# Kernel optimization log

Measured on AMD Instinct MI355X. Metric: run time of the kernel, lower is better.

The kernel has to match this reference:

```python
import jax, jax.numpy as jnp
import numpy as np

N = 50000      # nodes
E = 400000     # edges (before self-loops)
NFEAT = 256
NHID = 64
NHEAD = 8
NOUT = 128


def gat_conv(h, src, dst, W, attn_l, attn_r, bias, n, H, D):
    """DGL GATConv (eval mode: feat_drop/attn_drop are no-ops), negative_slope=0.2."""
    feat = (h @ W).reshape(n, H, D)                      # [N,H,D]
    el = jnp.einsum('nhd,hd->nh', feat, attn_l)          # [N,H]
    er = jnp.einsum('nhd,hd->nh', feat, attn_r)          # [N,H]
    e = jax.nn.leaky_relu(el[src] + er[dst], 0.2)        # [E,H]
    # segment softmax over incoming edges of each dst node
    m = jax.ops.segment_max(e, dst, num_segments=n)      # [N,H] (every node has a self-loop)
    ex = jnp.exp(e - m[dst])
    denom = jax.ops.segment_sum(ex, dst, num_segments=n)
    a = ex / denom[dst]                                  # [E,H]
    rst = jax.ops.segment_sum(a[:, :, None] * feat[src], dst, num_segments=n)  # [N,H,D]
    return rst + bias.reshape(1, H, D)


def setup_inputs() -> dict:
    key = jax.random.key(0)
    ks = jax.random.split(key, 10)
    s = 0.1
    x = jax.random.normal(ks[0], (N, NFEAT), jnp.float32)
    edge_index = jax.random.randint(ks[1], (2, E), 0, N, dtype=jnp.int64)
    W1 = jax.random.normal(ks[2], (NFEAT, NHEAD * NHID), jnp.float32) * s
    al1 = jax.random.normal(ks[3], (NHEAD, NHID), jnp.float32) * s
    ar1 = jax.random.normal(ks[4], (NHEAD, NHID), jnp.float32) * s
    b1 = jax.random.normal(ks[5], (NHEAD * NHID,), jnp.float32) * s
    W2 = jax.random.normal(ks[6], (NHEAD * NHID, NOUT), jnp.float32) * s
    al2 = jax.random.normal(ks[7], (1, NOUT), jnp.float32) * s
    ar2 = jax.random.normal(ks[8], (1, NOUT), jnp.float32) * s
    b2 = jax.random.normal(ks[9], (NOUT,), jnp.float32) * s
    return {"x": x, "edge_index": edge_index, "W1": W1, "al1": al1, "ar1": ar1,
            "b1": b1, "W2": W2, "al2": al2, "ar2": ar2, "b2": b2}


def reference(x, edge_index, W1, al1, ar1, b1, W2, al2, ar2, b2):
    n = x.shape[0]
    loop = jnp.arange(n, dtype=edge_index.dtype)
    src = jnp.concatenate([edge_index[0], loop])  # dgl.add_self_loop
    dst = jnp.concatenate([edge_index[1], loop])
    # hidden layer (dropout is identity in eval mode)
    h = gat_conv(x, src, dst, W1, al1, ar1, b1, n, NHEAD, NHID).reshape(n, NFEAT * 2)
    h = jax.nn.elu(h)
    out = gat_conv(h, src, dst, W2, al2, ar2, b2, n, 1, NOUT).reshape(n, NOUT)
    return out
```

## Files before the change

kernel.cpp:

```cpp
#include <hip/hip_runtime.h>

#define NFEAT 256
#define NHID 64
#define NHEAD 8
#define HID1 512
#define NOUT 128

typedef unsigned short ushort_t;
typedef unsigned int uint_t;
typedef __attribute__((ext_vector_type(8))) short short8;
typedef __attribute__((ext_vector_type(4))) float floatx4;
typedef __attribute__((ext_vector_type(4))) ushort_t ushort4_t;

static __device__ __forceinline__ float bf2f(uint_t s) {
    return __uint_as_float(s << 16);
}
static __device__ __forceinline__ ushort_t f2bf(float f) {
    uint_t u = __float_as_uint(f);
    u += 0x7FFF + ((u >> 16) & 1);
    return (ushort_t)(u >> 16);
}

__global__ void k_prep(const float* __restrict__ x, ushort_t* __restrict__ xb,
                       const float* __restrict__ W1, ushort_t* __restrict__ W1t,
                       const float* __restrict__ W2, ushort_t* __restrict__ W2t,
                       const int* __restrict__ dstA, int* __restrict__ deg,
                       int n, int E, int c0, int c1, int c2) {
    int blk = blockIdx.x;
    int t = threadIdx.x;
    if (blk < c0) {
        int i = blk * 256 + t;
        floatx4 f = ((const floatx4*)x)[i];
        ushort4_t o;
        #pragma unroll
        for (int j = 0; j < 4; ++j) o[j] = f2bf(f[j]);
        ((ushort4_t*)xb)[i] = o;
    } else if (blk < c1) {
        int i = (blk - c0) * 256 + t;
        int nn = i / NFEAT, kk = i % NFEAT;
        W1t[i] = f2bf(W1[(size_t)kk * HID1 + nn]);
    } else if (blk < c2) {
        int i = (blk - c1) * 256 + t;
        int nn = i / HID1, kk = i % HID1;
        W2t[i] = f2bf(W2[(size_t)kk * NOUT + nn]);
    } else {
        int i = (blk - c2) * 256 + t;
        if (i < E + n) {
            int d = (i < E) ? dstA[i] : (i - E);
            atomicAdd(&deg[d], 1);
        }
    }
}

__global__ __launch_bounds__(1024) void k_scan(const int* __restrict__ deg, int* __restrict__ indptr, int n) {
    __shared__ int part[1024];
    int t = threadIdx.x;
    int chunk = (n + 1023) >> 10;
    int b = t * chunk;
    int e = min(b + chunk, n);
    int s = 0;
    int i = b;
    for (; i + 3 < e; i += 4)
        s += (deg[i] + deg[i + 1]) + (deg[i + 2] + deg[i + 3]);
    for (; i < e; ++i) s += deg[i];
    part[t] = s;
    __syncthreads();
    for (int off = 1; off < 1024; off <<= 1) {
        int v = (t >= off) ? part[t - off] : 0;
        __syncthreads();
        part[t] += v;
        __syncthreads();
    }
    int run = (t == 0) ? 0 : part[t - 1];
    i = b;
    for (; i + 3 < e; i += 4) {
        int d0 = deg[i], d1 = deg[i + 1], d2 = deg[i + 2], d3 = deg[i + 3];
        indptr[i] = run; run += d0;
        indptr[i + 1] = run; run += d1;
        indptr[i + 2] = run; run += d2;
        indptr[i + 3] = run; run += d3;
    }
    for (; i < e; ++i) { indptr[i] = run; run += deg[i]; }
    if (t == 1023) indptr[n] = part[1023];
}

__global__ void k_fill(const int* __restrict__ srcA, const int* __restrict__ dstA, int E, int n,
                       const int* __restrict__ indptr, int* __restrict__ cnt,
                       int* __restrict__ csr_src, int* __restrict__ csr_dst) {
    int i = blockIdx.x * blockDim.x + threadIdx.x;
    if (i >= E + n) return;
    int s, d;
    if (i < E) { s = srcA[i]; d = dstA[i]; } else { s = i - E; d = s; }
    int pos = indptr[d] + atomicAdd(&cnt[d], 1);
    csr_src[pos] = s;
    csr_dst[pos] = d;
}

__global__ __launch_bounds__(256) void k_gemm1(const ushort_t* __restrict__ A,
                                               const ushort_t* __restrict__ Bt,
                                               ushort_t* __restrict__ C,
                                               const float* __restrict__ al,
                                               const float* __restrict__ ar,
                                               float* __restrict__ el, float* __restrict__ er,
                                               int M) {
    const int N = HID1, K = NFEAT;
    __shared__ __align__(16) ushort_t As[128 * 32];
    __shared__ __align__(16) ushort_t Bs[128 * 32];
    const int t = threadIdx.x;
    const int w = t >> 6, lane = t & 63;
    const int l16 = lane & 15, quad = lane >> 4;
    const int m0 = blockIdx.y * 128, n0 = blockIdx.x * 128;
    const int r0 = (w >> 1) * 64;
    const int c0 = (w & 1) * 64;

    floatx4 acc[4][4] = {};

    const int srow[2] = { (0 * 256 + t) >> 2, (1 * 256 + t) >> 2 };
    const int skp = (t & 3) * 8;
    const int wbase0 = (0 * 256 + (t & ~63)) * 8;
    const int wbase1 = (1 * 256 + (t & ~63)) * 8;

    for (int k0 = 0; k0 < K; k0 += 32) {
        int gr0 = m0 + srow[0]; if (gr0 >= M) gr0 = M - 1;
        int gr1 = m0 + srow[1]; if (gr1 >= M) gr1 = M - 1;
        const ushort_t* gpa0 = A + (size_t)gr0 * K + k0 + skp;
        const ushort_t* gpa1 = A + (size_t)gr1 * K + k0 + skp;
        const ushort_t* gpb0 = Bt + (size_t)(n0 + srow[0]) * K + k0 + skp;
        const ushort_t* gpb1 = Bt + (size_t)(n0 + srow[1]) * K + k0 + skp;
        __builtin_amdgcn_global_load_lds((const __attribute__((address_space(1))) void*)gpa0,
            (__attribute__((address_space(3))) void*)(As + wbase0), 16, 0, 0);
        __builtin_amdgcn_global_load_lds((const __attribute__((address_space(1))) void*)gpa1,
            (__attribute__((address_space(3))) void*)(As + wbase1), 16, 0, 0);
        __builtin_amdgcn_global_load_lds((const __attribute__((address_space(1))) void*)gpb0,
            (__attribute__((address_space(3))) void*)(Bs + wbase0), 16, 0, 0);
        __builtin_amdgcn_global_load_lds((const __attribute__((address_space(1))) void*)gpb1,
            (__attribute__((address_space(3))) void*)(Bs + wbase1), 16, 0, 0);
        __syncthreads();

        short8 af[4], bf[4];
        #pragma unroll
        for (int i = 0; i < 4; ++i)
            af[i] = *(const short8*)(As + (r0 + i * 16 + l16) * 32 + quad * 8);
        #pragma unroll
        for (int j = 0; j < 4; ++j)
            bf[j] = *(const short8*)(Bs + (c0 + j * 16 + l16) * 32 + quad * 8);
        #pragma unroll
        for (int i = 0; i < 4; ++i)
            #pragma unroll
            for (int j = 0; j < 4; ++j)
                acc[i][j] = __builtin_amdgcn_mfma_f32_16x16x32_bf16(af[i], bf[j], acc[i][j], 0, 0, 0);
        __syncthreads();
    }

    #pragma unroll
    for (int i = 0; i < 4; ++i) {
        #pragma unroll
        for (int r = 0; r < 4; ++r) {
            int row = m0 + r0 + i * 16 + quad * 4 + r;
            if (row < M) {
                #pragma unroll
                for (int j = 0; j < 4; ++j)
                    C[(size_t)row * N + n0 + c0 + j * 16 + l16] = f2bf(acc[i][j][r]);
            }
        }
    }

    float alv[4], arv[4];
    #pragma unroll
    for (int j = 0; j < 4; ++j) {
        int col = n0 + c0 + j * 16 + l16;
        alv[j] = al[col];
        arv[j] = ar[col];
    }
    int head = (n0 + c0) >> 6;
    #pragma unroll
    for (int i = 0; i < 4; ++i) {
        #pragma unroll
        for (int r = 0; r < 4; ++r) {
            float p = acc[i][0][r] * alv[0] + acc[i][1][r] * alv[1]
                    + acc[i][2][r] * alv[2] + acc[i][3][r] * alv[3];
            float q = acc[i][0][r] * arv[0] + acc[i][1][r] * arv[1]
                    + acc[i][2][r] * arv[2] + acc[i][3][r] * arv[3];
            #pragma unroll
            for (int o = 8; o > 0; o >>= 1) {
                p += __shfl_down(p, o);
                q += __shfl_down(q, o);
            }
            if (l16 == 0) {
                int row = m0 + r0 + i * 16 + quad * 4 + r;
                if (row < M) {
                    el[row * NHEAD + head] = p;
                    er[row * NHEAD + head] = q;
                }
            }
        }
    }
}

__global__ __launch_bounds__(256) void k_gemm2(const ushort_t* __restrict__ A,
                                               const ushort_t* __restrict__ Bt,
                                               ushort_t* __restrict__ C,
                                               const float* __restrict__ al,
                                               const float* __restrict__ ar,
                                               float* __restrict__ el, float* __restrict__ er,
                                               int M) {
    const int N = NOUT, K = HID1;
    __shared__ __align__(16) ushort_t As[64 * 32];
    __shared__ __align__(16) ushort_t Bs[128 * 32];
    __shared__ float elp[64][2], erp[64][2];
    const int t = threadIdx.x;
    const int w = t >> 6, lane = t & 63;
    const int l16 = lane & 15, quad = lane >> 4;
    const int m0 = blockIdx.y * 64;
    const int r0 = (w >> 1) * 32;
    const int c0 = (w & 1) * 64;

    floatx4 acc[2][4] = {};

    const int arow = t >> 2;
    const int brow[2] = { (0 * 256 + t) >> 2, (1 * 256 + t) >> 2 };
    const int skp = (t & 3) * 8;
    const int wbaseA = (t & ~63) * 8;
    const int wbase0 = (0 * 256 + (t & ~63)) * 8;
    const int wbase1 = (1 * 256 + (t & ~63)) * 8;

    for (int k0 = 0; k0 < K; k0 += 32) {
        int gr = m0 + arow; if (gr >= M) gr = M - 1;
        const ushort_t* gpa = A + (size_t)gr * K + k0 + skp;
        const ushort_t* gpb0 = Bt + (size_t)brow[0] * K + k0 + skp;
        const ushort_t* gpb1 = Bt + (size_t)brow[1] * K + k0 + skp;
        __builtin_amdgcn_global_load_lds((const __attribute__((address_space(1))) void*)gpa,
            (__attribute__((address_space(3))) void*)(As + wbaseA), 16, 0, 0);
        __builtin_amdgcn_global_load_lds((const __attribute__((address_space(1))) void*)gpb0,
            (__attribute__((address_space(3))) void*)(Bs + wbase0), 16, 0, 0);
        __builtin_amdgcn_global_load_lds((const __attribute__((address_space(1))) void*)gpb1,
            (__attribute__((address_space(3))) void*)(Bs + wbase1), 16, 0, 0);
        __syncthreads();

        short8 af[2], bf[4];
        #pragma unroll
        for (int i = 0; i < 2; ++i)
            af[i] = *(const short8*)(As + (r0 + i * 16 + l16) * 32 + quad * 8);
        #pragma unroll
        for (int j = 0; j < 4; ++j)
            bf[j] = *(const short8*)(Bs + (c0 + j * 16 + l16) * 32 + quad * 8);
        #pragma unroll
        for (int i = 0; i < 2; ++i)
            #pragma unroll
            for (int j = 0; j < 4; ++j)
                acc[i][j] = __builtin_amdgcn_mfma_f32_16x16x32_bf16(af[i], bf[j], acc[i][j], 0, 0, 0);
        __syncthreads();
    }

    float alv[4], arv[4];
    #pragma unroll
    for (int j = 0; j < 4; ++j) {
        int col = c0 + j * 16 + l16;
        alv[j] = al[col];
        arv[j] = ar[col];
    }
    #pragma unroll
    for (int i = 0; i < 2; ++i) {
        #pragma unroll
        for (int r = 0; r < 4; ++r) {
            int lrow = r0 + i * 16 + quad * 4 + r;
            int row = m0 + lrow;
            if (row < M) {
                #pragma unroll
                for (int j = 0; j < 4; ++j)
                    C[(size_t)row * N + c0 + j * 16 + l16] = f2bf(acc[i][j][r]);
            }
            float p = acc[i][0][r] * alv[0] + acc[i][1][r] * alv[1]
                    + acc[i][2][r] * alv[2] + acc[i][3][r] * alv[3];
            float q = acc[i][0][r] * arv[0] + acc[i][1][r] * arv[1]
                    + acc[i][2][r] * arv[2] + acc[i][3][r] * arv[3];
            #pragma unroll
            for (int o = 8; o > 0; o >>= 1) {
                p += __shfl_down(p, o);
                q += __shfl_down(q, o);
            }
            if (l16 == 0) {
                elp[lrow][w & 1] = p;
                erp[lrow][w & 1] = q;
            }
        }
    }
    __syncthreads();
    if (t < 64) {
        int row = m0 + t;
        if (row < M) {
            el[row] = elp[t][0] + elp[t][1];
            er[row] = erp[t][0] + erp[t][1];
        }
    }
}

__global__ void k_wgt1(const int* __restrict__ csr_src, const int* __restrict__ csr_dst,
                       const float* __restrict__ el, const float* __restrict__ er,
                       float* __restrict__ wcsr, int ET) {
    int idx = blockIdx.x * blockDim.x + threadIdx.x;
    if (idx >= ET * NHEAD) return;
    int e = idx >> 3, h = idx & 7;
    int s = csr_src[e], d = csr_dst[e];
    float x = el[s * NHEAD + h] + er[d * NHEAD + h];
    x = (x > 0.f) ? x : 0.2f * x;
    wcsr[idx] = __expf(x);
}

__global__ void k_wgt2(const int* __restrict__ csr_src, const int* __restrict__ csr_dst,
                       const float* __restrict__ el2, const float* __restrict__ er2,
                       float* __restrict__ wcsr, int ET) {
    int e = blockIdx.x * blockDim.x + threadIdx.x;
    if (e >= ET) return;
    int s = csr_src[e], d = csr_dst[e];
    float x = el2[s] + er2[d];
    x = (x > 0.f) ? x : 0.2f * x;
    wcsr[e] = __expf(x);
}

__global__ __launch_bounds__(256) void k_agg1(const uint_t* __restrict__ fb, const float* __restrict__ wcsr,
                                              const float* __restrict__ b1,
                                              const int* __restrict__ indptr, const int* __restrict__ csr_src,
                                              uint_t* __restrict__ h1b, int n) {
    int node = blockIdx.x;
    int t = threadIdx.x;
    int h = t >> 5;
    int e0 = indptr[node], e1 = indptr[node + 1];
    float a0 = 0.f, a1 = 0.f, den = 0.f;
    int e = e0;
    for (; e + 3 < e1; e += 4) {
        int s0 = csr_src[e], s1 = csr_src[e + 1], s2 = csr_src[e + 2], s3 = csr_src[e + 3];
        float w0 = wcsr[(size_t)e * NHEAD + h];
        float w1 = wcsr[(size_t)(e + 1) * NHEAD + h];
        float w2 = wcsr[(size_t)(e + 2) * NHEAD + h];
        float w3 = wcsr[(size_t)(e + 3) * NHEAD + h];
        uint_t u0 = fb[(size_t)s0 * 256 + t];
        uint_t u1 = fb[(size_t)s1 * 256 + t];
        uint_t u2 = fb[(size_t)s2 * 256 + t];
        uint_t u3 = fb[(size_t)s3 * 256 + t];
        den += (w0 + w1) + (w2 + w3);
        a0 += w0 * bf2f(u0 & 0xFFFF) + w1 * bf2f(u1 & 0xFFFF)
            + w2 * bf2f(u2 & 0xFFFF) + w3 * bf2f(u3 & 0xFFFF);
        a1 += w0 * bf2f(u0 >> 16) + w1 * bf2f(u1 >> 16)
            + w2 * bf2f(u2 >> 16) + w3 * bf2f(u3 >> 16);
    }
    for (; e < e1; ++e) {
        int s = csr_src[e];
        float w = wcsr[(size_t)e * NHEAD + h];
        uint_t u = fb[(size_t)s * 256 + t];
        den += w;
        a0 += w * bf2f(u & 0xFFFF);
        a1 += w * bf2f(u >> 16);
    }
    float inv = 1.f / den;
    float v0 = a0 * inv + b1[2 * t];
    float v1 = a1 * inv + b1[2 * t + 1];
    v0 = (v0 > 0.f) ? v0 : (__expf(v0) - 1.f);
    v1 = (v1 > 0.f) ? v1 : (__expf(v1) - 1.f);
    h1b[(size_t)node * 256 + t] = (uint_t)f2bf(v0) | ((uint_t)f2bf(v1) << 16);
}

__global__ __launch_bounds__(256) void k_agg2(const uint_t* __restrict__ fb2, const float* __restrict__ wcsr,
                                              const float* __restrict__ b2,
                                              const int* __restrict__ indptr, const int* __restrict__ csr_src,
                                              float* __restrict__ out, int n) {
    int wid = blockIdx.x * 4 + (threadIdx.x >> 6);
    int lane = threadIdx.x & 63;
    if (wid >= n) return;
    int e0 = indptr[wid], e1 = indptr[wid + 1];
    float a0 = 0.f, a1 = 0.f, den = 0.f;
    int e = e0;
    for (; e + 3 < e1; e += 4) {
        int s0 = csr_src[e], s1 = csr_src[e + 1], s2 = csr_src[e + 2], s3 = csr_src[e + 3];
        float w0 = wcsr[e], w1 = wcsr[e + 1], w2 = wcsr[e + 2], w3 = wcsr[e + 3];
        uint_t u0 = fb2[(size_t)s0 * 64 + lane];
        uint_t u1 = fb2[(size_t)s1 * 64 + lane];
        uint_t u2 = fb2[(size_t)s2 * 64 + lane];
        uint_t u3 = fb2[(size_t)s3 * 64 + lane];
        den += (w0 + w1) + (w2 + w3);
        a0 += w0 * bf2f(u0 & 0xFFFF) + w1 * bf2f(u1 & 0xFFFF)
            + w2 * bf2f(u2 & 0xFFFF) + w3 * bf2f(u3 & 0xFFFF);
        a1 += w0 * bf2f(u0 >> 16) + w1 * bf2f(u1 >> 16)
            + w2 * bf2f(u2 >> 16) + w3 * bf2f(u3 >> 16);
    }
    for (; e < e1; ++e) {
        int s = csr_src[e];
        float w = wcsr[e];
        uint_t u = fb2[(size_t)s * 64 + lane];
        den += w;
        a0 += w * bf2f(u & 0xFFFF);
        a1 += w * bf2f(u >> 16);
    }
    float inv = 1.f / den;
    float2 o;
    o.x = a0 * inv + b2[2 * lane];
    o.y = a1 * inv + b2[2 * lane + 1];
    ((float2*)out)[(size_t)wid * 64 + lane] = o;
}

extern "C" void kernel_launch(void* const* d_in, const int* in_sizes, int n_in,
                              void* d_out, int out_size, void* d_ws, size_t ws_size,
                              hipStream_t stream) {
    const float* x   = (const float*)d_in[0];
    const int*   ei  = (const int*)d_in[1];
    const float* W1  = (const float*)d_in[2];
    const float* al1 = (const float*)d_in[3];
    const float* ar1 = (const float*)d_in[4];
    const float* b1  = (const float*)d_in[5];
    const float* W2  = (const float*)d_in[6];
    const float* al2 = (const float*)d_in[7];
    const float* ar2 = (const float*)d_in[8];
    const float* b2  = (const float*)d_in[9];

    const int n  = in_sizes[0] / NFEAT;
    const int E  = in_sizes[1] / 2;
    const int ET = E + n;
    const int* srcA = ei;
    const int* dstA = ei + E;

    char* ws = (char*)d_ws;
    size_t off = 0;
    auto alloc = [&](size_t bytes) -> void* {
        void* p = ws + off;
        off += (bytes + 255) & ~(size_t)255;
        return p;
    };
    ushort_t* xb     = (ushort_t*)alloc((size_t)n * NFEAT * 2);
    ushort_t* feat1b = (ushort_t*)alloc((size_t)n * HID1 * 2);
    ushort_t* h1b    = (ushort_t*)alloc((size_t)n * HID1 * 2);
    ushort_t* feat2b = (ushort_t*)alloc((size_t)n * NOUT * 2);
    ushort_t* W1t    = (ushort_t*)alloc((size_t)NFEAT * HID1 * 2);
    ushort_t* W2t    = (ushort_t*)alloc((size_t)HID1 * NOUT * 2);
    float* el1 = (float*)alloc((size_t)n * NHEAD * 4);
    float* er1 = (float*)alloc((size_t)n * NHEAD * 4);
    float* el2 = (float*)alloc((size_t)n * 4);
    float* er2 = (float*)alloc((size_t)n * 4);
    float* wcsr1 = (float*)alloc((size_t)ET * NHEAD * 4);
    float* wcsr2 = (float*)alloc((size_t)ET * 4);
    int* indptr  = (int*)alloc((size_t)(n + 1) * 4);
    int* deg     = (int*)alloc((size_t)n * 4);
    int* cnt     = (int*)alloc((size_t)n * 4);
    int* csr     = (int*)alloc((size_t)ET * 4);
    int* csrd    = (int*)alloc((size_t)ET * 4);

    hipMemsetAsync(deg, 0, (size_t)n * 4, stream);
    hipMemsetAsync(cnt, 0, (size_t)n * 4, stream);

    const int c0 = (n * NFEAT / 4) / 256;
    const int c1 = c0 + (NFEAT * HID1) / 256;
    const int c2 = c1 + (HID1 * NOUT) / 256;
    const int c3 = c2 + (ET + 255) / 256;
    k_prep<<<c3, 256, 0, stream>>>(x, xb, W1, W1t, W2, W2t, dstA, deg, n, E, c0, c1, c2);

    k_scan<<<1, 1024, 0, stream>>>(deg, indptr, n);
    k_fill<<<(ET + 255) / 256, 256, 0, stream>>>(srcA, dstA, E, n, indptr, cnt, csr, csrd);

    k_gemm1<<<dim3(HID1 / 128, (n + 127) / 128), 256, 0, stream>>>(xb, W1t, feat1b, al1, ar1, el1, er1, n);
    k_wgt1<<<(ET * NHEAD + 255) / 256, 256, 0, stream>>>(csr, csrd, el1, er1, wcsr1, ET);
    k_agg1<<<n, 256, 0, stream>>>((const uint_t*)feat1b, wcsr1, b1, indptr, csr, (uint_t*)h1b, n);

    k_gemm2<<<dim3(1, (n + 63) / 64), 256, 0, stream>>>(h1b, W2t, feat2b, al2, ar2, el2, er2, n);
    k_wgt2<<<(ET + 255) / 256, 256, 0, stream>>>(csr, csrd, el2, er2, wcsr2, ET);
    k_agg2<<<(n + 3) / 4, 256, 0, stream>>>((const uint_t*)feat2b, wcsr2, b2, indptr, csr, (float*)d_out, n);
}
```

Before: 386.7 us.

## Fuse edge-weight computation into aggregation kernels and widen GEMM1 tile

Removes the separate k_wgt1/k_wgt2 kernels and the csr_dst array. Edge attention weights are now computed on the fly inside k_agg1 and k_agg2, staged through shared memory in chunks, which avoids writing and re-reading per-edge weight buffers. GEMM1 now uses a 128x256 tile, so each wave produces two heads' el/er, and the two memsets are merged into one. The cost is extra shared-memory syncs per chunk, more accumulator registers in GEMM1 that may lower occupancy, and exp work that now sits inside the aggregation kernels.

Result: no change. 387.0 us (+0.1%).

```diff
diff --git a/kernel.cpp b/kernel.cpp
--- a/kernel.cpp
+++ b/kernel.cpp
@@ -86,14 +86,13 @@
 
 __global__ void k_fill(const int* __restrict__ srcA, const int* __restrict__ dstA, int E, int n,
                        const int* __restrict__ indptr, int* __restrict__ cnt,
-                       int* __restrict__ csr_src, int* __restrict__ csr_dst) {
+                       int* __restrict__ csr_src) {
     int i = blockIdx.x * blockDim.x + threadIdx.x;
     if (i >= E + n) return;
     int s, d;
     if (i < E) { s = srcA[i]; d = dstA[i]; } else { s = i - E; d = s; }
     int pos = indptr[d] + atomicAdd(&cnt[d], 1);
     csr_src[pos] = s;
-    csr_dst[pos] = d;
 }
 
 __global__ __launch_bounds__(256) void k_gemm1(const ushort_t* __restrict__ A,
@@ -105,49 +104,46 @@
                                                int M) {
     const int N = HID1, K = NFEAT;
     __shared__ __align__(16) ushort_t As[128 * 32];
-    __shared__ __align__(16) ushort_t Bs[128 * 32];
+    __shared__ __align__(16) ushort_t Bs[256 * 32];
     const int t = threadIdx.x;
     const int w = t >> 6, lane = t & 63;
     const int l16 = lane & 15, quad = lane >> 4;
-    const int m0 = blockIdx.y * 128, n0 = blockIdx.x * 128;
+    const int m0 = blockIdx.y * 128, n0 = blockIdx.x * 256;
     const int r0 = (w >> 1) * 64;
-    const int c0 = (w & 1) * 64;
-
-    floatx4 acc[4][4] = {};
-
-    const int srow[2] = { (0 * 256 + t) >> 2, (1 * 256 + t) >> 2 };
+    const int c0 = (w & 1) * 128;
+
+    floatx4 acc[4][8] = {};
+
     const int skp = (t & 3) * 8;
-    const int wbase0 = (0 * 256 + (t & ~63)) * 8;
-    const int wbase1 = (1 * 256 + (t & ~63)) * 8;
-
     for (int k0 = 0; k0 < K; k0 += 32) {
-        int gr0 = m0 + srow[0]; if (gr0 >= M) gr0 = M - 1;
-        int gr1 = m0 + srow[1]; if (gr1 >= M) gr1 = M - 1;
-        const ushort_t* gpa0 = A + (size_t)gr0 * K + k0 + skp;
-        const ushort_t* gpa1 = A + (size_t)gr1 * K + k0 + skp;
-        const ushort_t* gpb0 = Bt + (size_t)(n0 + srow[0]) * K + k0 + skp;
-        const ushort_t* gpb1 = Bt + (size_t)(n0 + srow[1]) * K + k0 + skp;
-        __builtin_amdgcn_global_load_lds((const __attribute__((address_space(1))) void*)gpa0,
-            (__attribute__((address_space(3))) void*)(As + wbase0), 16, 0, 0);
-        __builtin_amdgcn_global_load_lds((const __attribute__((address_space(1))) void*)gpa1,
-            (__attribute__((address_space(3))) void*)(As + wbase1), 16, 0, 0);
-        __builtin_amdgcn_global_load_lds((const __attribute__((address_space(1))) void*)gpb0,
-            (__attribute__((address_space(3))) void*)(Bs + wbase0), 16, 0, 0);
-        __builtin_amdgcn_global_load_lds((const __attribute__((address_space(1))) void*)gpb1,
-            (__attribute__((address_space(3))) void*)(Bs + wbase1), 16, 0, 0);
-        __syncthreads();
-
-        short8 af[4], bf[4];
+        #pragma unroll
+        for (int j = 0; j < 2; ++j) {
+            int r = (j * 256 + t) >> 2;
+            int gr = m0 + r; if (gr >= M) gr = M - 1;
+            const ushort_t* gp = A + (size_t)gr * K + k0 + skp;
+            __builtin_amdgcn_global_load_lds((const __attribute__((address_space(1))) void*)gp,
+                (__attribute__((address_space(3))) void*)(As + (j * 256 + (t & ~63)) * 8), 16, 0, 0);
+        }
+        #pragma unroll
+        for (int j = 0; j < 4; ++j) {
+            int r = (j * 256 + t) >> 2;
+            const ushort_t* gp = Bt + (size_t)(n0 + r) * K + k0 + skp;
+            __builtin_amdgcn_global_load_lds((const __attribute__((address_space(1))) void*)gp,
+                (__attribute__((address_space(3))) void*)(Bs + (j * 256 + (t & ~63)) * 8), 16, 0, 0);
+        }
+        __syncthreads();
+
+        short8 af[4], bf[8];
         #pragma unroll
         for (int i = 0; i < 4; ++i)
             af[i] = *(const short8*)(As + (r0 + i * 16 + l16) * 32 + quad * 8);
         #pragma unroll
-        for (int j = 0; j < 4; ++j)
+        for (int j = 0; j < 8; ++j)
             bf[j] = *(const short8*)(Bs + (c0 + j * 16 + l16) * 32 + quad * 8);
         #pragma unroll
         for (int i = 0; i < 4; ++i)
             #pragma unroll
-            for (int j = 0; j < 4; ++j)
+            for (int j = 0; j < 8; ++j)
                 acc[i][j] = __builtin_amdgcn_mfma_f32_16x16x32_bf16(af[i], bf[j], acc[i][j], 0, 0, 0);
         __syncthreads();
     }
@@ -159,38 +155,46 @@
             int row = m0 + r0 + i * 16 + quad * 4 + r;
             if (row < M) {
                 #pragma unroll
-                for (int j = 0; j < 4; ++j)
+                for (int j = 0; j < 8; ++j)
                     C[(size_t)row * N + n0 + c0 + j * 16 + l16] = f2bf(acc[i][j][r]);
             }
         }
     }
 
-    float alv[4], arv[4];
+    float alv[8], arv[8];
     #pragma unroll
-    for (int j = 0; j < 4; ++j) {
+    for (int j = 0; j < 8; ++j) {
         int col = n0 + c0 + j * 16 + l16;
         alv[j] = al[col];
         arv[j] = ar[col];
     }
-    int head = (n0 + c0) >> 6;
+    int head0 = (n0 + c0) >> 6;
     #pragma unroll
     for (int i = 0; i < 4; ++i) {
         #pragma unroll
         for (int r = 0; r < 4; ++r) {
-            float p = acc[i][0][r] * alv[0] + acc[i][1][r] * alv[1]
-                    + acc[i][2][r] * alv[2] + acc[i][3][r] * alv[3];
-            float q = acc[i][0][r] * arv[0] + acc[i][1][r] * arv[1]
-                    + acc[i][2][r] * arv[2] + acc[i][3][r] * arv[3];
+            float pa = acc[i][0][r] * alv[0] + acc[i][1][r] * alv[1]
+                     + acc[i][2][r] * alv[2] + acc[i][3][r] * alv[3];
+            float qa = acc[i][0][r] * arv[0] + acc[i][1][r] * arv[1]
+                     + acc[i][2][r] * arv[2] + acc[i][3][r] * arv[3];
+            float pb = acc[i][4][r] * alv[4] + acc[i][5][r] * alv[5]
+                     + acc[i][6][r] * alv[6] + acc[i][7][r] * alv[7];
+            float qb = acc[i][4][r] * arv[4] + acc[i][5][r] * arv[5]
+                     + acc[i][6][r] * arv[6] + acc[i][7][r] * arv[7];
             #pragma unroll
             for (int o = 8; o > 0; o >>= 1) {
-                p += __shfl_down(p, o);
-                q += __shfl_down(q, o);
+                pa += __shfl_down(pa, o);
+                qa += __shfl_down(qa, o);
+                pb += __shfl_down(pb, o);
+                qb += __shfl_down(qb, o);
             }
             if (l16 == 0) {
                 int row = m0 + r0 + i * 16 + quad * 4 + r;
                 if (row < M) {
-                    el[row * NHEAD + head] = p;
-                    er[row * NHEAD + head] = q;
+                    el[row * NHEAD + head0] = pa;
+                    er[row * NHEAD + head0] = qa;
+                    el[row * NHEAD + head0 + 1] = pb;
+                    er[row * NHEAD + head0 + 1] = qb;
                 }
             }
         }
@@ -218,23 +222,21 @@
     floatx4 acc[2][4] = {};
 
     const int arow = t >> 2;
-    const int brow[2] = { (0 * 256 + t) >> 2, (1 * 256 + t) >> 2 };
     const int skp = (t & 3) * 8;
     const int wbaseA = (t & ~63) * 8;
-    const int wbase0 = (0 * 256 + (t & ~63)) * 8;
-    const int wbase1 = (1 * 256 + (t & ~63)) * 8;
 
     for (int k0 = 0; k0 < K; k0 += 32) {
         int gr = m0 + arow; if (gr >= M) gr = M - 1;
         const ushort_t* gpa = A + (size_t)gr * K + k0 + skp;
-        const ushort_t* gpb0 = Bt + (size_t)brow[0] * K + k0 + skp;
-        const ushort_t* gpb1 = Bt + (size_t)brow[1] * K + k0 + skp;
         __builtin_amdgcn_global_load_lds((const __attribute__((address_space(1))) void*)gpa,
             (__attribute__((address_space(3))) void*)(As + wbaseA), 16, 0, 0);
-        __builtin_amdgcn_global_load_lds((const __attribute__((address_space(1))) void*)gpb0,
-            (__attribute__((address_space(3))) void*)(Bs + wbase0), 16, 0, 0);
-        __builtin_amdgcn_global_load_lds((const __attribute__((address_space(1))) void*)gpb1,
-            (__attribute__((address_space(3))) void*)(Bs + wbase1), 16, 0, 0);
+        #pragma unroll
+        for (int j = 0; j < 2; ++j) {
+            int r = (j * 256 + t) >> 2;
+            const ushort_t* gpb = Bt + (size_t)r * K + k0 + skp;
+            __builtin_amdgcn_global_load_lds((const __attribute__((address_space(1))) void*)gpb,
+                (__attribute__((address_space(3))) void*)(Bs + (j * 256 + (t & ~63)) * 8), 16, 0, 0);
+        }
         __syncthreads();
 
         short8 af[2], bf[4];
@@ -295,63 +297,58 @@
     }
 }
 
-__global__ void k_wgt1(const int* __restrict__ csr_src, const int* __restrict__ csr_dst,
-                       const float* __restrict__ el, const float* __restrict__ er,
-                       float* __restrict__ wcsr, int ET) {
-    int idx = blockIdx.x * blockDim.x + threadIdx.x;
-    if (idx >= ET * NHEAD) return;
-    int e = idx >> 3, h = idx & 7;
-    int s = csr_src[e], d = csr_dst[e];
-    float x = el[s * NHEAD + h] + er[d * NHEAD + h];
-    x = (x > 0.f) ? x : 0.2f * x;
-    wcsr[idx] = __expf(x);
-}
-
-__global__ void k_wgt2(const int* __restrict__ csr_src, const int* __restrict__ csr_dst,
-                       const float* __restrict__ el2, const float* __restrict__ er2,
-                       float* __restrict__ wcsr, int ET) {
-    int e = blockIdx.x * blockDim.x + threadIdx.x;
-    if (e >= ET) return;
-    int s = csr_src[e], d = csr_dst[e];
-    float x = el2[s] + er2[d];
-    x = (x > 0.f) ? x : 0.2f * x;
-    wcsr[e] = __expf(x);
-}
-
-__global__ __launch_bounds__(256) void k_agg1(const uint_t* __restrict__ fb, const float* __restrict__ wcsr,
+__global__ __launch_bounds__(256) void k_agg1(const uint_t* __restrict__ fb,
+                                              const float* __restrict__ el, const float* __restrict__ er,
                                               const float* __restrict__ b1,
                                               const int* __restrict__ indptr, const int* __restrict__ csr_src,
                                               uint_t* __restrict__ h1b, int n) {
+    __shared__ float wch[32 * 8];
+    __shared__ int sch[32];
     int node = blockIdx.x;
     int t = threadIdx.x;
     int h = t >> 5;
+    int et = t >> 3, hw = t & 7;
     int e0 = indptr[node], e1 = indptr[node + 1];
+    int deg = e1 - e0;
+    float erv = er[node * NHEAD + hw];
     float a0 = 0.f, a1 = 0.f, den = 0.f;
-    int e = e0;
-    for (; e + 3 < e1; e += 4) {
-        int s0 = csr_src[e], s1 = csr_src[e + 1], s2 = csr_src[e + 2], s3 = csr_src[e + 3];
-        float w0 = wcsr[(size_t)e * NHEAD + h];
-        float w1 = wcsr[(size_t)(e + 1) * NHEAD + h];
-        float w2 = wcsr[(size_t)(e + 2) * NHEAD + h];
-        float w3 = wcsr[(size_t)(e + 3) * NHEAD + h];
-        uint_t u0 = fb[(size_t)s0 * 256 + t];
-        uint_t u1 = fb[(size_t)s1 * 256 + t];
-        uint_t u2 = fb[(size_t)s2 * 256 + t];
-        uint_t u3 = fb[(size_t)s3 * 256 + t];
-        den += (w0 + w1) + (w2 + w3);
-        a0 += w0 * bf2f(u0 & 0xFFFF) + w1 * bf2f(u1 & 0xFFFF)
-            + w2 * bf2f(u2 & 0xFFFF) + w3 * bf2f(u3 & 0xFFFF);
-        a1 += w0 * bf2f(u0 >> 16) + w1 * bf2f(u1 >> 16)
-            + w2 * bf2f(u2 >> 16) + w3 * bf2f(u3 >> 16);
-    }
-    for (; e < e1; ++e) {
-        int s = csr_src[e];
-        float w = wcsr[(size_t)e * NHEAD + h];
-        uint_t u = fb[(size_t)s * 256 + t];
-        den += w;
-        a0 += w * bf2f(u & 0xFFFF);
-        a1 += w * bf2f(u >> 16);
-    }
+
+    for (int base = 0; base < deg; base += 32) {
+        int cnt = min(32, deg - base);
+        if (et < cnt) {
+            int s = csr_src[e0 + base + et];
+            if (hw == 0) sch[et] = s;
+            float x = el[s * NHEAD + hw] + erv;
+            x = (x > 0.f) ? x : 0.2f * x;
+            wch[et * 8 + hw] = __expf(x);
+        }
+        __syncthreads();
+        int e = 0;
+        for (; e + 3 < cnt; e += 4) {
+            int s0 = sch[e], s1 = sch[e + 1], s2 = sch[e + 2], s3 = sch[e + 3];
+            float w0 = wch[e * 8 + h], w1 = wch[(e + 1) * 8 + h];
+            float w2 = wch[(e + 2) * 8 + h], w3 = wch[(e + 3) * 8 + h];
+            uint_t u0 = fb[(size_t)s0 * 256 + t];
+            uint_t u1 = fb[(size_t)s1 * 256 + t];
+            uint_t u2 = fb[(size_t)s2 * 256 + t];
+            uint_t u3 = fb[(size_t)s3 * 256 + t];
+            den += (w0 + w1) + (w2 + w3);
+            a0 += w0 * bf2f(u0 & 0xFFFF) + w1 * bf2f(u1 & 0xFFFF)
+                + w2 * bf2f(u2 & 0xFFFF) + w3 * bf2f(u3 & 0xFFFF);
+            a1 += w0 * bf2f(u0 >> 16) + w1 * bf2f(u1 >> 16)
+                + w2 * bf2f(u2 >> 16) + w3 * bf2f(u3 >> 16);
+        }
+        for (; e < cnt; ++e) {
+            int s = sch[e];
+            float ww = wch[e * 8 + h];
+            uint_t u = fb[(size_t)s * 256 + t];
+            den += ww;
+            a0 += ww * bf2f(u & 0xFFFF);
+            a1 += ww * bf2f(u >> 16);
+        }
+        __syncthreads();
+    }
+
     float inv = 1.f / den;
     float v0 = a0 * inv + b1[2 * t];
     float v1 = a1 * inv + b1[2 * t + 1];
@@ -360,37 +357,57 @@
     h1b[(size_t)node * 256 + t] = (uint_t)f2bf(v0) | ((uint_t)f2bf(v1) << 16);
 }
 
-__global__ __launch_bounds__(256) void k_agg2(const uint_t* __restrict__ fb2, const float* __restrict__ wcsr,
+__global__ __launch_bounds__(256) void k_agg2(const uint_t* __restrict__ fb2,
+                                              const float* __restrict__ el2, const float* __restrict__ er2,
                                               const float* __restrict__ b2,
                                               const int* __restrict__ indptr, const int* __restrict__ csr_src,
                                               float* __restrict__ out, int n) {
-    int wid = blockIdx.x * 4 + (threadIdx.x >> 6);
+    __shared__ float wch[4][64];
+    __shared__ int sch[4][64];
+    int w = threadIdx.x >> 6;
+    int wid = blockIdx.x * 4 + w;
     int lane = threadIdx.x & 63;
     if (wid >= n) return;
+    float erv = er2[wid];
     int e0 = indptr[wid], e1 = indptr[wid + 1];
+    int deg = e1 - e0;
     float a0 = 0.f, a1 = 0.f, den = 0.f;
-    int e = e0;
-    for (; e + 3 < e1; e += 4) {
-        int s0 = csr_src[e], s1 = csr_src[e + 1], s2 = csr_src[e + 2], s3 = csr_src[e + 3];
-        float w0 = wcsr[e], w1 = wcsr[e + 1], w2 = wcsr[e + 2], w3 = wcsr[e + 3];
-        uint_t u0 = fb2[(size_t)s0 * 64 + lane];
-        uint_t u1 = fb2[(size_t)s1 * 64 + lane];
-        uint_t u2 = fb2[(size_t)s2 * 64 + lane];
-        uint_t u3 = fb2[(size_t)s3 * 64 + lane];
-        den += (w0 + w1) + (w2 + w3);
-        a0 += w0 * bf2f(u0 & 0xFFFF) + w1 * bf2f(u1 & 0xFFFF)
-            + w2 * bf2f(u2 & 0xFFFF) + w3 * bf2f(u3 & 0xFFFF);
-        a1 += w0 * bf2f(u0 >> 16) + w1 * bf2f(u1 >> 16)
-            + w2 * bf2f(u2 >> 16) + w3 * bf2f(u3 >> 16);
-    }
-    for (; e < e1; ++e) {
-        int s = csr_src[e];
-        float w = wcsr[e];
-        uint_t u = fb2[(size_t)s * 64 + lane];
-        den += w;
-        a0 += w * bf2f(u & 0xFFFF);
-        a1 += w * bf2f(u >> 16);
-    }
+
+    for (int base = 0; base < deg; base += 64) {
+        int cnt = min(64, deg - base);
+        if (lane < cnt) {
+            int s = csr_src[e0 + base + lane];
+            sch[w][lane] = s;
+            float x = el2[s] + erv;
+            x = (x > 0.f) ? x : 0.2f * x;
+            wch[w][lane] = __expf(x);
+        }
+        __builtin_amdgcn_wave_barrier();
+        int e = 0;
+        for (; e + 3 < cnt; e += 4) {
+            int s0 = sch[w][e], s1 = sch[w][e + 1], s2 = sch[w][e + 2], s3 = sch[w][e + 3];
+            float w0 = wch[w][e], w1 = wch[w][e + 1], w2 = wch[w][e + 2], w3 = wch[w][e + 3];
+            uint_t u0 = fb2[(size_t)s0 * 64 + lane];
+            uint_t u1 = fb2[(size_t)s1 * 64 + lane];
+            uint_t u2 = fb2[(size_t)s2 * 64 + lane];
+            uint_t u3 = fb2[(size_t)s3 * 64 + lane];
+            den += (w0 + w1) + (w2 + w3);
+            a0 += w0 * bf2f(u0 & 0xFFFF) + w1 * bf2f(u1 & 0xFFFF)
+                + w2 * bf2f(u2 & 0xFFFF) + w3 * bf2f(u3 & 0xFFFF);
+            a1 += w0 * bf2f(u0 >> 16) + w1 * bf2f(u1 >> 16)
+                + w2 * bf2f(u2 >> 16) + w3 * bf2f(u3 >> 16);
+        }
+        for (; e < cnt; ++e) {
+            int s = sch[w][e];
+            float ww = wch[w][e];
+            uint_t u = fb2[(size_t)s * 64 + lane];
+            den += ww;
+            a0 += ww * bf2f(u & 0xFFFF);
+            a1 += ww * bf2f(u >> 16);
+        }
+        __builtin_amdgcn_wave_barrier();
+    }
+
     float inv = 1.f / den;
     float2 o;
     o.x = a0 * inv + b2[2 * lane];
@@ -435,16 +452,12 @@
     float* er1 = (float*)alloc((size_t)n * NHEAD * 4);
     float* el2 = (float*)alloc((size_t)n * 4);
     float* er2 = (float*)alloc((size_t)n * 4);
-    float* wcsr1 = (float*)alloc((size_t)ET * NHEAD * 4);
-    float* wcsr2 = (float*)alloc((size_t)ET * 4);
-    int* indptr  = (int*)alloc((size_t)(n + 1) * 4);
-    int* deg     = (int*)alloc((size_t)n * 4);
-    int* cnt     = (int*)alloc((size_t)n * 4);
-    int* csr     = (int*)alloc((size_t)ET * 4);
-    int* csrd    = (int*)alloc((size_t)ET * 4);
-
-    hipMemsetAsync(deg, 0, (size_t)n * 4, stream);
-    hipMemsetAsync(cnt, 0, (size_t)n * 4, stream);
+    int* indptr = (int*)alloc((size_t)(n + 1) * 4);
+    int* deg    = (int*)alloc((size_t)2 * n * 4);
+    int* cnt    = deg + n;
+    int* csr    = (int*)alloc((size_t)ET * 4);
+
+    hipMemsetAsync(deg, 0, (size_t)2 * n * 4, stream);
 
     const int c0 = (n * NFEAT / 4) / 256;
     const int c1 = c0 + (NFEAT * HID1) / 256;
@@ -453,13 +466,11 @@
     k_prep<<<c3, 256, 0, stream>>>(x, xb, W1, W1t, W2, W2t, dstA, deg, n, E, c0, c1, c2);
 
     k_scan<<<1, 1024, 0, stream>>>(deg, indptr, n);
-    k_fill<<<(ET + 255) / 256, 256, 0, stream>>>(srcA, dstA, E, n, indptr, cnt, csr, csrd);
-
-    k_gemm1<<<dim3(HID1 / 128, (n + 127) / 128), 256, 0, stream>>>(xb, W1t, feat1b, al1, ar1, el1, er1, n);
-    k_wgt1<<<(ET * NHEAD + 255) / 256, 256, 0, stream>>>(csr, csrd, el1, er1, wcsr1, ET);
-    k_agg1<<<n, 256, 0, stream>>>((const uint_t*)feat1b, wcsr1, b1, indptr, csr, (uint_t*)h1b, n);
+    k_fill<<<(ET + 255) / 256, 256, 0, stream>>>(srcA, dstA, E, n, indptr, cnt, csr);
+
+    k_gemm1<<<dim3(HID1 / 256, (n + 127) / 128), 256, 0, stream>>>(xb, W1t, feat1b, al1, ar1, el1, er1, n);
+    k_agg1<<<n, 256, 0, stream>>>((const uint_t*)feat1b, el1, er1, b1, indptr, csr, (uint_t*)h1b, n);
 
     k_gemm2<<<dim3(1, (n + 63) / 64), 256, 0, stream>>>(h1b, W2t, feat2b, al2, ar2, el2, er2, n);
-    k_wgt2<<<(ET + 255) / 256, 256, 0, stream>>>(csr, csrd, el2, er2, wcsr2, ET);
-    k_agg2<<<(n + 3) / 4, 256, 0, stream>>>((const uint_t*)feat2b, wcsr2, b2, indptr, csr, (float*)d_out, n);
-}
+    k_agg2<<<(n + 3) / 4, 256, 0, stream>>>((const uint_t*)feat2b, el2, er2, b2, indptr, csr, (float*)d_out, n);
+}
```
